# Optimization experiments

Measured on AMD Instinct MI355X. Metric: run time of the kernel, lower is better.

## Reference

```python
import jax, jax.numpy as jnp
import numpy as np

NUM_HEADS = 16
EMBED_DIM = 1024
LN_EPS = 1e-5


def setup_inputs() -> dict:
    key = jax.random.key(0)
    ks = jax.random.split(key, 9)
    B, S, D = 4, 1024, EMBED_DIM
    return {
        "query": jax.random.normal(ks[0], (B, S, D), dtype=jnp.float32),
        "key": jax.random.normal(ks[1], (B, S, D), dtype=jnp.float32),
        "value": jax.random.normal(ks[2], (B, S, D), dtype=jnp.float32),
        "W_query": 0.01 * jax.random.normal(ks[3], (D, D), dtype=jnp.float32),
        "W_key": 0.01 * jax.random.normal(ks[4], (D, D), dtype=jnp.float32),
        "W_value": 0.01 * jax.random.normal(ks[5], (D, D), dtype=jnp.float32),
        "W_output": 0.01 * jax.random.normal(ks[6], (D, D), dtype=jnp.float32),
        "ln_gamma": jnp.ones((D,), dtype=jnp.float32),
        "ln_beta": jnp.zeros((D,), dtype=jnp.float32),
        "mask": 1,
    }


def _split_heads(x):
    # [B,S,D] -> [H,B,S,d]; torch split(dim=-1)+stack(dim=0) gives head h = cols h*d:(h+1)*d
    B, S, D = x.shape
    d = D // NUM_HEADS
    return jnp.moveaxis(x.reshape(B, S, NUM_HEADS, d), 2, 0)


def reference(query, key, value, W_query, W_key, W_value, W_output, ln_gamma, ln_beta, mask):
    B, S, D = query.shape
    d = D // NUM_HEADS
    q = _split_heads(query @ W_query)   # [H,B,S,d]
    k = _split_heads(key @ W_key)       # [H,B,S,d]
    v = _split_heads(value @ W_value)   # [H,B,S,d]
    scale = jnp.asarray(np.sqrt(d), dtype=q.dtype)
    scores = jnp.einsum("hbqd,hbkd->hbqk", q, k) / scale  # [H,B,S,S]
    attn = jax.nn.softmax(scores, axis=-1)
    if mask:
        # post-hoc causal: zero strict upper triangle, then renormalize rows
        tri = jnp.tril(jnp.ones((S, S), dtype=bool))
        attn = jnp.where(tri, attn, 0.0)
        attn = attn / jnp.sum(attn, axis=-1, keepdims=True)
    ws = jnp.einsum("hbqk,hbkd->hbqd", attn, v)            # [H,B,S,d]
    concat = jnp.moveaxis(ws, 0, 2).reshape(B, S, D)       # [B,S,D]
    out = concat @ W_output + query                        # residual
    mu = jnp.mean(out, axis=-1, keepdims=True)
    var = jnp.var(out, axis=-1, keepdims=True)
    out = (out - mu) / jnp.sqrt(var + LN_EPS) * ln_gamma + ln_beta
    return out, attn
```

## Files before the change

kernel.cpp:

```cpp
#include <hip/hip_runtime.h>
#include <hip/hip_bf16.h>

#define Bn   4
#define Sn   1024
#define Dn   1024
#define Hn   16
#define dHn  64
#define HB   (Hn * Bn)
#define MROWS (Bn * Sn)
#define QNE  ((size_t)Bn * Sn * Dn)

typedef __attribute__((ext_vector_type(8))) short bf16x8;
typedef __attribute__((ext_vector_type(4))) float f32x4;

__device__ __forceinline__ ushort f2bf(float x) {
  union { float f; unsigned u; } v; v.f = x;
  unsigned r = v.u + 0x7FFF + ((v.u >> 16) & 1);
  return (ushort)(r >> 16);
}
__device__ __forceinline__ float bf2f(ushort u) {
  union { unsigned u; float f; } v; v.u = ((unsigned)u) << 16; return v.f;
}

__device__ __forceinline__ void load_lds16(const void* g, void* l) {
  __builtin_amdgcn_global_load_lds(
      (const __attribute__((address_space(1))) unsigned int*)g,
      (__attribute__((address_space(3))) unsigned int*)l, 16, 0, 0);
}

__global__ __launch_bounds__(256) void cast3_kernel(
    const float* __restrict__ q, const float* __restrict__ k,
    const float* __restrict__ v, ushort* __restrict__ outb) {
  const float* in = blockIdx.y == 0 ? q : (blockIdx.y == 1 ? k : v);
  ushort* out = outb + (size_t)blockIdx.y * QNE;
  int idx = blockIdx.x * 256 + threadIdx.x;
  float4 x = *(const float4*)&in[(size_t)idx * 4];
  ushort4 o;
  o.x = f2bf(x.x); o.y = f2bf(x.y); o.z = f2bf(x.z); o.w = f2bf(x.w);
  *(ushort4*)&out[(size_t)idx * 4] = o;
}

__global__ __launch_bounds__(256) void transpose4_kernel(
    const float* __restrict__ Wq, const float* __restrict__ Wk,
    const float* __restrict__ Wv, const float* __restrict__ Wo,
    ushort* __restrict__ WTb) {
  const int z = blockIdx.z;
  const float* W = z == 0 ? Wq : (z == 1 ? Wk : (z == 2 ? Wv : Wo));
  ushort* WT = WTb + (size_t)z * Dn * Dn;
  __shared__ ushort T[64 * 72];
  const int k0 = blockIdx.y * 64, n0 = blockIdx.x * 64;
  const int t = threadIdx.x;
  const int r = t >> 4, c4 = (t & 15) * 4;
#pragma unroll
  for (int i = 0; i < 4; ++i) {
    int row = r + i * 16;
    float4 v = *(const float4*)&W[(size_t)(k0 + row) * Dn + n0 + c4];
    T[(c4 + 0) * 72 + row] = f2bf(v.x);
    T[(c4 + 1) * 72 + row] = f2bf(v.y);
    T[(c4 + 2) * 72 + row] = f2bf(v.z);
    T[(c4 + 3) * 72 + row] = f2bf(v.w);
  }
  __syncthreads();
#pragma unroll
  for (int i = 0; i < 2; ++i) {
    int c = t + i * 256;
    int n = c >> 3, kg = (c & 7) * 8;
    *(ulonglong2*)&WT[(size_t)(n0 + n) * Dn + k0 + kg] =
        *(const ulonglong2*)&T[n * 72 + kg];
  }
}

__global__ __launch_bounds__(256, 3) void qkv_gemm(
    const ushort* __restrict__ Ab, const ushort* __restrict__ Bb,
    ushort* __restrict__ Cb) {
  const int z = blockIdx.z;
  const ushort* A  = Ab + (size_t)z * QNE;
  const ushort* Bt = Bb + (size_t)z * Dn * Dn;
  ushort* C        = Cb + (size_t)z * QNE;
  const int N = Dn, K = Dn;

  __shared__ ushort lds[17408];
  ushort* As = lds;
  ushort* Bs = lds + 4096;
  const int t = threadIdx.x;
  const int w = t >> 6, lane = t & 63;
  const int wr = (w >> 1) * 64, wc = (w & 1) * 64;
  const int l16 = lane & 15, quad = lane >> 4;
  const int flat = blockIdx.y * 8 + blockIdx.x;
  const int nf = (flat & 7) * 32 + (flat >> 3);
  const int m0 = (nf >> 3) * 128, n0 = (nf & 7) * 128;
  const int srow = (lane >> 2);
  const int scol = (lane & 3) * 8;
  f32x4 acc[4][4] = {};
  for (int k0 = 0; k0 < K; k0 += 32) {
#pragma unroll
    for (int c = 0; c < 2; ++c) {
      int row = w * 32 + c * 16 + srow;
      load_lds16(&A[(size_t)(m0 + row) * K + k0 + scol],
                 &As[(size_t)w * 1024 + c * 512]);
      load_lds16(&Bt[(size_t)(n0 + row) * K + k0 + scol],
                 &Bs[(size_t)w * 1024 + c * 512]);
    }
    __syncthreads();
    bf16x8 af[4], bfr[4];
#pragma unroll
    for (int mi = 0; mi < 4; ++mi)
      af[mi] = *(const bf16x8*)&As[(wr + mi * 16 + l16) * 32 + quad * 8];
#pragma unroll
    for (int ni = 0; ni < 4; ++ni)
      bfr[ni] = *(const bf16x8*)&Bs[(wc + ni * 16 + l16) * 32 + quad * 8];
#pragma unroll
    for (int mi = 0; mi < 4; ++mi)
#pragma unroll
      for (int ni = 0; ni < 4; ++ni)
        acc[mi][ni] = __builtin_amdgcn_mfma_f32_16x16x32_bf16(
            af[mi], bfr[ni], acc[mi][ni], 0, 0, 0);
    __syncthreads();
  }
  if (z == 2) {
    ushort* Cs = lds;
#pragma unroll
    for (int mi = 0; mi < 4; ++mi)
#pragma unroll
      for (int ni = 0; ni < 4; ++ni) {
        int col = wc + ni * 16 + l16;
#pragma unroll
        for (int r = 0; r < 4; ++r)
          Cs[col * 136 + wr + mi * 16 + quad * 4 + r] = f2bf(acc[mi][ni][r]);
      }
    __syncthreads();
    const int b = m0 >> 10, s0 = m0 & 1023;
#pragma unroll
    for (int i = 0; i < 8; ++i) {
      int c = t + i * 256;
      int nl = c >> 4, mg = (c & 15) * 8;
      *(ulonglong2*)&C[((size_t)b * Dn + n0 + nl) * Sn + s0 + mg] =
          *(const ulonglong2*)&Cs[nl * 136 + mg];
    }
  } else {
    ushort* Cs = lds;
#pragma unroll
    for (int mi = 0; mi < 4; ++mi)
#pragma unroll
      for (int ni = 0; ni < 4; ++ni) {
        int col = wc + ni * 16 + l16;
#pragma unroll
        for (int r = 0; r < 4; ++r)
          Cs[(wr + mi * 16 + quad * 4 + r) * 136 + col] = f2bf(acc[mi][ni][r]);
      }
    __syncthreads();
#pragma unroll
    for (int i = 0; i < 8; ++i) {
      int c = t + i * 256;
      int row = c >> 4, cg = (c & 15) * 8;
      *(ulonglong2*)&C[(size_t)(m0 + row) * N + n0 + cg] =
          *(const ulonglong2*)&Cs[row * 136 + cg];
    }
  }
}

__global__ __launch_bounds__(256, 3) void gemm_out(
    const ushort* __restrict__ A, const ushort* __restrict__ Bt,
    const float* __restrict__ resid, float* __restrict__ C,
    int M, int N, int K) {
  __shared__ ushort lds[6144];
  ushort* As = lds;
  ushort* Bs = lds + 4096;
  const int t = threadIdx.x;
  const int w = t >> 6, lane = t & 63;
  const int wr = (w >> 1) * 64, wc = (w & 1) * 32;
  const int l16 = lane & 15, quad = lane >> 4;
  const int f = blockIdx.y * 16 + blockIdx.x;
  const int idx = f >> 3;
  const int m0 = ((f & 7) * 4 + (idx >> 4)) * 128;
  const int n0 = (idx & 15) * 64;
  const int srow = (lane >> 2);
  const int scol = (lane & 3) * 8;
  f32x4 acc[4][2] = {};
  for (int k0 = 0; k0 < K; k0 += 32) {
#pragma unroll
    for (int c = 0; c < 2; ++c) {
      int row = w * 32 + c * 16 + srow;
      load_lds16(&A[(size_t)(m0 + row) * K + k0 + scol],
                 &As[(size_t)w * 1024 + c * 512]);
    }
    load_lds16(&Bt[(size_t)(n0 + w * 16 + srow) * K + k0 + scol],
               &Bs[(size_t)w * 512]);
    __syncthreads();
    bf16x8 af[4], bfr[2];
#pragma unroll
    for (int mi = 0; mi < 4; ++mi)
      af[mi] = *(const bf16x8*)&As[(wr + mi * 16 + l16) * 32 + quad * 8];
#pragma unroll
    for (int ni = 0; ni < 2; ++ni)
      bfr[ni] = *(const bf16x8*)&Bs[(wc + ni * 16 + l16) * 32 + quad * 8];
#pragma unroll
    for (int mi = 0; mi < 4; ++mi)
#pragma unroll
      for (int ni = 0; ni < 2; ++ni)
        acc[mi][ni] = __builtin_amdgcn_mfma_f32_16x16x32_bf16(
            af[mi], bfr[ni], acc[mi][ni], 0, 0, 0);
    __syncthreads();
  }
#pragma unroll
  for (int mi = 0; mi < 4; ++mi)
#pragma unroll
    for (int ni = 0; ni < 2; ++ni) {
      int n = n0 + wc + ni * 16 + l16;
#pragma unroll
      for (int r = 0; r < 4; ++r) {
        int m = m0 + wr + mi * 16 + quad * 4 + r;
        float v = acc[mi][ni][r];
        v += resid[(size_t)m * N + n];
        C[(size_t)m * N + n] = v;
      }
    }
}

__global__ __launch_bounds__(256, 3) void attn_fused(
    const ushort* __restrict__ Qp, const ushort* __restrict__ Kp,
    const ushort* __restrict__ Vt, float* __restrict__ attn,
    ushort* __restrict__ Cc) {
  const int hb = blockIdx.x, qt = (gridDim.y - 1) - blockIdx.y;
  const int h = hb >> 2, b = hb & 3;
  const int q0 = qt * 64;
  const int nkt = (qt >> 1) + 1;

  __shared__ ushort Ks[128 * 72];
  __shared__ ushort Vs[64 * 136];
  __shared__ ushort Ps[64 * 136];
  __shared__ float lds_inv[64];

  const int t = threadIdx.x;
  const int w = t >> 6, lane = t & 63;
  const int l16 = lane & 15, quad = lane >> 4;

  for (int ktz = nkt; ktz < 8; ++ktz) {
    const int k0 = ktz * 128;
#pragma unroll
    for (int i = 0; i < 4; ++i) {
      int cc = t + i * 256;
      int row = cc >> 4, cg = (cc & 15) * 8;
      float* dst = &attn[((size_t)hb * Sn + q0 + row) * Sn + k0 + cg];
      *(float4*)&dst[0] = make_float4(0.f, 0.f, 0.f, 0.f);
      *(float4*)&dst[4] = make_float4(0.f, 0.f, 0.f, 0.f);
    }
  }

  bf16x8 aq[2];
#pragma unroll
  for (int ks = 0; ks < 2; ++ks)
    aq[ks] = *(const bf16x8*)&Qp[((size_t)b * Sn + q0 + w * 16 + l16) * Dn +
                                 h * dHn + ks * 32 + quad * 8];

  float l_run[4] = {0.f, 0.f, 0.f, 0.f};

  for (int kt = 0; kt < nkt; ++kt) {
    const int k0 = kt * 128;
    const bool halfT = (kt == nkt - 1) && ((qt & 1) == 0);
    const int nni = halfT ? 4 : 8;
    const int kiters = halfT ? 2 : 4;
#pragma unroll
    for (int i = 0; i < 4; ++i) {
      if (i < kiters) {
        int cc = t + i * 256;
        int row = cc >> 3, cg = (cc & 7) * 8;
        *(ulonglong2*)&Ks[row * 72 + cg] =
            *(const ulonglong2*)&Kp[((size_t)b * Sn + k0 + row) * Dn + h * dHn + cg];
      }
    }
    __syncthreads();
    f32x4 s[8];
#pragma unroll
    for (int ni = 0; ni < 8; ++ni) {
      if (ni < nni) {
        f32x4 a = {};
#pragma unroll
        for (int ks = 0; ks < 2; ++ks) {
          bf16x8 bk = *(const bf16x8*)&Ks[(ni * 16 + l16) * 72 + ks * 32 + quad * 8];
          a = __builtin_amdgcn_mfma_f32_16x16x32_bf16(aq[ks], bk, a, 0, 0, 0);
        }
        s[ni] = a;
      }
    }
    float tsum[4] = {0.f, 0.f, 0.f, 0.f};
#pragma unroll
    for (int ni = 0; ni < 8; ++ni) {
      if (ni < nni)
#pragma unroll
        for (int r = 0; r < 4; ++r) {
          int kg = k0 + ni * 16 + l16;
          int qg = q0 + w * 16 + quad * 4 + r;
          float e = __expf(s[ni][r] * 0.125f);
          tsum[r] += (kg <= qg) ? e : 0.f;
        }
    }
#pragma unroll
    for (int d = 1; d < 16; d <<= 1)
#pragma unroll
      for (int r = 0; r < 4; ++r) tsum[r] += __shfl_xor(tsum[r], d);
#pragma unroll
    for (int r = 0; r < 4; ++r) l_run[r] += tsum[r];
    __syncthreads();
  }
  float inv_l[4];
#pragma unroll
  for (int r = 0; r < 4; ++r) inv_l[r] = 1.0f / l_run[r];
  if (l16 == 0)
#pragma unroll
    for (int r = 0; r < 4; ++r) lds_inv[w * 16 + quad * 4 + r] = inv_l[r];
  __syncthreads();

  f32x4 acc_o[4] = {};
  for (int kt = 0; kt < nkt; ++kt) {
    const int k0 = kt * 128;
    const bool halfT = (kt == nkt - 1) && ((qt & 1) == 0);
    const int nni = halfT ? 4 : 8;
    const int kiters = halfT ? 2 : 4;
    const int nks = halfT ? 2 : 4;
#pragma unroll
    for (int i = 0; i < 4; ++i) {
      if (i < kiters) {
        int cc = t + i * 256;
        int row = cc >> 3, cg = (cc & 7) * 8;
        *(ulonglong2*)&Ks[row * 72 + cg] =
            *(const ulonglong2*)&Kp[((size_t)b * Sn + k0 + row) * Dn + h * dHn + cg];
      }
    }
    if (halfT) {
#pragma unroll
      for (int i = 0; i < 2; ++i) {
        int cc = t + i * 256;
        int row = cc >> 3, cg = (cc & 7) * 8;
        *(ulonglong2*)&Vs[row * 136 + cg] =
            *(const ulonglong2*)&Vt[((size_t)b * Dn + h * dHn + row) * Sn + k0 + cg];
      }
    } else {
#pragma unroll
      for (int i = 0; i < 4; ++i) {
        int cc = t + i * 256;
        int row = cc >> 4, cg = (cc & 15) * 8;
        *(ulonglong2*)&Vs[row * 136 + cg] =
            *(const ulonglong2*)&Vt[((size_t)b * Dn + h * dHn + row) * Sn + k0 + cg];
      }
    }
    __syncthreads();
    f32x4 s[8];
#pragma unroll
    for (int ni = 0; ni < 8; ++ni) {
      if (ni < nni) {
        f32x4 a = {};
#pragma unroll
        for (int ks = 0; ks < 2; ++ks) {
          bf16x8 bk = *(const bf16x8*)&Ks[(ni * 16 + l16) * 72 + ks * 32 + quad * 8];
          a = __builtin_amdgcn_mfma_f32_16x16x32_bf16(aq[ks], bk, a, 0, 0, 0);
        }
        s[ni] = a;
      }
    }
#pragma unroll
    for (int ni = 0; ni < 8; ++ni)
#pragma unroll
      for (int r = 0; r < 4; ++r) {
        int pd = (w * 16 + quad * 4 + r) * 136 + ni * 16 + l16;
        float p = 0.f;
        if (ni < nni) {
          int kg = k0 + ni * 16 + l16;
          int qg = q0 + w * 16 + quad * 4 + r;
          float e = __expf(s[ni][r] * 0.125f);
          p = (kg <= qg) ? e : 0.f;
        }
        Ps[pd] = f2bf(p);
      }
#pragma unroll
    for (int ks = 0; ks < 4; ++ks) {
      if (ks < nks) {
        bf16x8 ap = *(const bf16x8*)&Ps[(w * 16 + l16) * 136 + ks * 32 + quad * 8];
#pragma unroll
        for (int ni = 0; ni < 4; ++ni) {
          bf16x8 bv = *(const bf16x8*)&Vs[(ni * 16 + l16) * 136 + ks * 32 + quad * 8];
          acc_o[ni] = __builtin_amdgcn_mfma_f32_16x16x32_bf16(ap, bv, acc_o[ni], 0, 0, 0);
        }
      }
    }
    __syncthreads();
#pragma unroll
    for (int i = 0; i < 4; ++i) {
      int cc = t + i * 256;
      int row = cc >> 4, cg = (cc & 15) * 8;
      float inv = lds_inv[row];
      bf16x8 pv = *(const bf16x8*)&Ps[row * 136 + cg];
      float* dst = &attn[((size_t)hb * Sn + q0 + row) * Sn + k0 + cg];
      *(float4*)&dst[0] = make_float4(bf2f((ushort)pv[0]) * inv, bf2f((ushort)pv[1]) * inv,
                                      bf2f((ushort)pv[2]) * inv, bf2f((ushort)pv[3]) * inv);
      *(float4*)&dst[4] = make_float4(bf2f((ushort)pv[4]) * inv, bf2f((ushort)pv[5]) * inv,
                                      bf2f((ushort)pv[6]) * inv, bf2f((ushort)pv[7]) * inv);
    }
  }
#pragma unroll
  for (int ni = 0; ni < 4; ++ni)
#pragma unroll
    for (int r = 0; r < 4; ++r) {
      int q = q0 + w * 16 + quad * 4 + r;
      int j = ni * 16 + l16;
      Cc[((size_t)b * Sn + q) * Dn + h * dHn + j] = f2bf(acc_o[ni][r] * inv_l[r]);
    }
}

__global__ __launch_bounds__(256) void ln_kernel(
    float* __restrict__ out, const float* __restrict__ gamma,
    const float* __restrict__ beta) {
  const int row = blockIdx.x;
  float* p = out + (size_t)row * Dn;
  const int t = threadIdx.x;
  float4 x = *(const float4*)&p[t * 4];
  float s  = x.x + x.y + x.z + x.w;
  float s2 = x.x * x.x + x.y * x.y + x.z * x.z + x.w * x.w;
#pragma unroll
  for (int d = 1; d < 64; d <<= 1) {
    s  += __shfl_xor(s, d);
    s2 += __shfl_xor(s2, d);
  }
  __shared__ float a1[4], a2[4];
  const int w = t >> 6, lane = t & 63;
  if (lane == 0) { a1[w] = s; a2[w] = s2; }
  __syncthreads();
  s  = a1[0] + a1[1] + a1[2] + a1[3];
  s2 = a2[0] + a2[1] + a2[2] + a2[3];
  const float mu  = s * (1.0f / Dn);
  const float var = s2 * (1.0f / Dn) - mu * mu;
  const float rstd = rsqrtf(var + 1e-5f);
  float4 g  = *(const float4*)&gamma[t * 4];
  float4 be = *(const float4*)&beta[t * 4];
  float4 o;
  o.x = (x.x - mu) * rstd * g.x + be.x;
  o.y = (x.y - mu) * rstd * g.y + be.y;
  o.z = (x.z - mu) * rstd * g.z + be.z;
  o.w = (x.w - mu) * rstd * g.w + be.w;
  *(float4*)&p[t * 4] = o;
}

extern "C" void kernel_launch(void* const* d_in, const int* in_sizes, int n_in,
                              void* d_out, int out_size, void* d_ws, size_t ws_size,
                              hipStream_t stream) {
  const float* q_in  = (const float*)d_in[0];
  const float* k_in  = (const float*)d_in[1];
  const float* v_in  = (const float*)d_in[2];
  const float* Wq    = (const float*)d_in[3];
  const float* Wk    = (const float*)d_in[4];
  const float* Wv    = (const float*)d_in[5];
  const float* Wo    = (const float*)d_in[6];
  const float* gamma = (const float*)d_in[7];
  const float* beta  = (const float*)d_in[8];

  float* out  = (float*)d_out;
  float* attn = out + (size_t)Bn * Sn * Dn;

  ushort* ws  = (ushort*)d_ws;
  ushort* qbf = ws;
  ushort* kbf = qbf + QNE;
  ushort* vbf = kbf + QNE;
  ushort* WqT = vbf + QNE;
  ushort* WkT = WqT + (size_t)Dn * Dn;
  ushort* WvT = WkT + (size_t)Dn * Dn;
  ushort* WoT = WvT + (size_t)Dn * Dn;
  ushort* Qp  = WoT + (size_t)Dn * Dn;
  ushort* Kp  = Qp + QNE;
  ushort* Vt  = Kp + QNE;
  ushort* Cc  = Vt + QNE;

  (void)kbf; (void)vbf; (void)WkT; (void)WvT; (void)Kp;

  cast3_kernel<<<dim3(QNE / 1024, 3), 256, 0, stream>>>(q_in, k_in, v_in, qbf);
  transpose4_kernel<<<dim3(Dn / 64, Dn / 64, 4), 256, 0, stream>>>(Wq, Wk, Wv, Wo, WqT);

  qkv_gemm<<<dim3(Dn / 128, MROWS / 128, 3), 256, 0, stream>>>(qbf, WqT, Qp);

  attn_fused<<<dim3(HB, Sn / 64), 256, 0, stream>>>(Qp, Kp, Vt, attn, Cc);

  gemm_out<<<dim3(Dn / 64, MROWS / 128), 256, 0, stream>>>(Cc, WoT, q_in, out, MROWS, Dn, Dn);
  ln_kernel<<<MROWS, 256, 0, stream>>>(out, gamma, beta);
}
```

Measured before the change: 445.6 us.

## Prefetch K/V tiles into registers, use nontemporal attn stores, and raise MFMA priority

Both passes of the attention kernel now load the next K (and V) tile into registers while the current tile is being computed, then write it to LDS at the start of the next iteration. This hides global load latency behind the MFMA work. Stores of the large fp32 attention matrix, both the zero fill and the probabilities, now use nontemporal stores to reduce cache pollution. s_setprio is raised around the MFMA sections. In exchange, the kernel holds more registers for kreg/vreg, which may lower occupancy.

```diff
diff --git a/kernel.cpp b/kernel.cpp
--- a/kernel.cpp
+++ b/kernel.cpp
@@ -242,8 +242,9 @@
       int cc = t + i * 256;
       int row = cc >> 4, cg = (cc & 15) * 8;
       float* dst = &attn[((size_t)hb * Sn + q0 + row) * Sn + k0 + cg];
-      *(float4*)&dst[0] = make_float4(0.f, 0.f, 0.f, 0.f);
-      *(float4*)&dst[4] = make_float4(0.f, 0.f, 0.f, 0.f);
+      f32x4 zz = {0.f, 0.f, 0.f, 0.f};
+      __builtin_nontemporal_store(zz, (f32x4*)&dst[0]);
+      __builtin_nontemporal_store(zz, (f32x4*)&dst[4]);
     }
   }
 
@@ -254,23 +255,44 @@
                                  h * dHn + ks * 32 + quad * 8];
 
   float l_run[4] = {0.f, 0.f, 0.f, 0.f};
-
+  ulonglong2 kreg[4], vreg[4];
+
+  {
+    const int ki0 = (nkt == 1 && (qt & 1) == 0) ? 2 : 4;
+#pragma unroll
+    for (int i = 0; i < 4; ++i)
+      if (i < ki0) {
+        int cc = t + i * 256;
+        int row = cc >> 3, cg = (cc & 7) * 8;
+        kreg[i] = *(const ulonglong2*)&Kp[((size_t)b * Sn + row) * Dn + h * dHn + cg];
+      }
+  }
   for (int kt = 0; kt < nkt; ++kt) {
     const int k0 = kt * 128;
     const bool halfT = (kt == nkt - 1) && ((qt & 1) == 0);
     const int nni = halfT ? 4 : 8;
     const int kiters = halfT ? 2 : 4;
 #pragma unroll
-    for (int i = 0; i < 4; ++i) {
+    for (int i = 0; i < 4; ++i)
       if (i < kiters) {
         int cc = t + i * 256;
         int row = cc >> 3, cg = (cc & 7) * 8;
-        *(ulonglong2*)&Ks[row * 72 + cg] =
-            *(const ulonglong2*)&Kp[((size_t)b * Sn + k0 + row) * Dn + h * dHn + cg];
-      }
-    }
-    __syncthreads();
+        *(ulonglong2*)&Ks[row * 72 + cg] = kreg[i];
+      }
+    __syncthreads();
+    if (kt + 1 < nkt) {
+      const int k0n = (kt + 1) * 128;
+      const int kiN = ((kt + 1 == nkt - 1) && ((qt & 1) == 0)) ? 2 : 4;
+#pragma unroll
+      for (int i = 0; i < 4; ++i)
+        if (i < kiN) {
+          int cc = t + i * 256;
+          int row = cc >> 3, cg = (cc & 7) * 8;
+          kreg[i] = *(const ulonglong2*)&Kp[((size_t)b * Sn + k0n + row) * Dn + h * dHn + cg];
+        }
+    }
     f32x4 s[8];
+    __builtin_amdgcn_s_setprio(1);
 #pragma unroll
     for (int ni = 0; ni < 8; ++ni) {
       if (ni < nni) {
@@ -283,6 +305,7 @@
         s[ni] = a;
       }
     }
+    __builtin_amdgcn_s_setprio(0);
     float tsum[4] = {0.f, 0.f, 0.f, 0.f};
 #pragma unroll
     for (int ni = 0; ni < 8; ++ni) {
@@ -309,6 +332,33 @@
   if (l16 == 0)
 #pragma unroll
     for (int r = 0; r < 4; ++r) lds_inv[w * 16 + quad * 4 + r] = inv_l[r];
+
+  {
+    const bool h0 = (nkt == 1) && ((qt & 1) == 0);
+    const int ki0 = h0 ? 2 : 4;
+#pragma unroll
+    for (int i = 0; i < 4; ++i)
+      if (i < ki0) {
+        int cc = t + i * 256;
+        int row = cc >> 3, cg = (cc & 7) * 8;
+        kreg[i] = *(const ulonglong2*)&Kp[((size_t)b * Sn + row) * Dn + h * dHn + cg];
+      }
+    if (h0) {
+#pragma unroll
+      for (int i = 0; i < 2; ++i) {
+        int cc = t + i * 256;
+        int row = cc >> 3, cg = (cc & 7) * 8;
+        vreg[i] = *(const ulonglong2*)&Vt[((size_t)b * Dn + h * dHn + row) * Sn + cg];
+      }
+    } else {
+#pragma unroll
+      for (int i = 0; i < 4; ++i) {
+        int cc = t + i * 256;
+        int row = cc >> 4, cg = (cc & 15) * 8;
+        vreg[i] = *(const ulonglong2*)&Vt[((size_t)b * Dn + h * dHn + row) * Sn + cg];
+      }
+    }
+  }
   __syncthreads();
 
   f32x4 acc_o[4] = {};
@@ -319,33 +369,57 @@
     const int kiters = halfT ? 2 : 4;
     const int nks = halfT ? 2 : 4;
 #pragma unroll
-    for (int i = 0; i < 4; ++i) {
+    for (int i = 0; i < 4; ++i)
       if (i < kiters) {
         int cc = t + i * 256;
         int row = cc >> 3, cg = (cc & 7) * 8;
-        *(ulonglong2*)&Ks[row * 72 + cg] =
-            *(const ulonglong2*)&Kp[((size_t)b * Sn + k0 + row) * Dn + h * dHn + cg];
-      }
-    }
+        *(ulonglong2*)&Ks[row * 72 + cg] = kreg[i];
+      }
     if (halfT) {
 #pragma unroll
       for (int i = 0; i < 2; ++i) {
         int cc = t + i * 256;
         int row = cc >> 3, cg = (cc & 7) * 8;
-        *(ulonglong2*)&Vs[row * 136 + cg] =
-            *(const ulonglong2*)&Vt[((size_t)b * Dn + h * dHn + row) * Sn + k0 + cg];
+        *(ulonglong2*)&Vs[row * 136 + cg] = vreg[i];
       }
     } else {
 #pragma unroll
       for (int i = 0; i < 4; ++i) {
         int cc = t + i * 256;
         int row = cc >> 4, cg = (cc & 15) * 8;
-        *(ulonglong2*)&Vs[row * 136 + cg] =
-            *(const ulonglong2*)&Vt[((size_t)b * Dn + h * dHn + row) * Sn + k0 + cg];
-      }
-    }
-    __syncthreads();
+        *(ulonglong2*)&Vs[row * 136 + cg] = vreg[i];
+      }
+    }
+    __syncthreads();
+    if (kt + 1 < nkt) {
+      const int k0n = (kt + 1) * 128;
+      const bool hN = (kt + 1 == nkt - 1) && ((qt & 1) == 0);
+      const int kiN = hN ? 2 : 4;
+#pragma unroll
+      for (int i = 0; i < 4; ++i)
+        if (i < kiN) {
+          int cc = t + i * 256;
+          int row = cc >> 3, cg = (cc & 7) * 8;
+          kreg[i] = *(const ulonglong2*)&Kp[((size_t)b * Sn + k0n + row) * Dn + h * dHn + cg];
+        }
+      if (hN) {
+#pragma unroll
+        for (int i = 0; i < 2; ++i) {
+          int cc = t + i * 256;
+          int row = cc >> 3, cg = (cc & 7) * 8;
+          vreg[i] = *(const ulonglong2*)&Vt[((size_t)b * Dn + h * dHn + row) * Sn + k0n + cg];
+        }
+      } else {
+#pragma unroll
+        for (int i = 0; i < 4; ++i) {
+          int cc = t + i * 256;
+          int row = cc >> 4, cg = (cc & 15) * 8;
+          vreg[i] = *(const ulonglong2*)&Vt[((size_t)b * Dn + h * dHn + row) * Sn + k0n + cg];
+        }
+      }
+    }
     f32x4 s[8];
+    __builtin_amdgcn_s_setprio(1);
 #pragma unroll
     for (int ni = 0; ni < 8; ++ni) {
       if (ni < nni) {
@@ -358,6 +432,7 @@
         s[ni] = a;
       }
     }
+    __builtin_amdgcn_s_setprio(0);
 #pragma unroll
     for (int ni = 0; ni < 8; ++ni)
 #pragma unroll
@@ -372,6 +447,7 @@
         }
         Ps[pd] = f2bf(p);
       }
+    __builtin_amdgcn_s_setprio(1);
 #pragma unroll
     for (int ks = 0; ks < 4; ++ks) {
       if (ks < nks) {
@@ -383,6 +459,7 @@
         }
       }
     }
+    __builtin_amdgcn_s_setprio(0);
     __syncthreads();
 #pragma unroll
     for (int i = 0; i < 4; ++i) {
@@ -391,10 +468,12 @@
       float inv = lds_inv[row];
       bf16x8 pv = *(const bf16x8*)&Ps[row * 136 + cg];
       float* dst = &attn[((size_t)hb * Sn + q0 + row) * Sn + k0 + cg];
-      *(float4*)&dst[0] = make_float4(bf2f((ushort)pv[0]) * inv, bf2f((ushort)pv[1]) * inv,
-                                      bf2f((ushort)pv[2]) * inv, bf2f((ushort)pv[3]) * inv);
-      *(float4*)&dst[4] = make_float4(bf2f((ushort)pv[4]) * inv, bf2f((ushort)pv[5]) * inv,
-                                      bf2f((ushort)pv[6]) * inv, bf2f((ushort)pv[7]) * inv);
+      f32x4 o0 = {bf2f((ushort)pv[0]) * inv, bf2f((ushort)pv[1]) * inv,
+                  bf2f((ushort)pv[2]) * inv, bf2f((ushort)pv[3]) * inv};
+      f32x4 o1 = {bf2f((ushort)pv[4]) * inv, bf2f((ushort)pv[5]) * inv,
+                  bf2f((ushort)pv[6]) * inv, bf2f((ushort)pv[7]) * inv};
+      __builtin_nontemporal_store(o0, (f32x4*)&dst[0]);
+      __builtin_nontemporal_store(o1, (f32x4*)&dst[4]);
     }
   }
 #pragma unroll
```

Result: slower. 511.3 us (+14.7%).
